# Optimization experiments

Hardware: AMD Instinct MI355X
Metric: run time of the kernel (lower is better)

Reference implementation:

```python
import jax, jax.numpy as jnp
import numpy as np

N_NODES = 10000; N_EDGES = 320000; D_NODE = 32; D_RAD = 8; D_SPH = 9
DIMS = (1, 3, 5); OFFS = (0, 1, 4); NI = 3; M = 8; HD = 16; LAT = 64; NL = 2; EPS = 1e-5
IDX = np.repeat(np.arange(NI), DIMS)  # irrep index per spherical-harmonic component
WN_ENV = NI * M            # 24  MakeWeightedChannels weight_numel
WN_LIN = NI * M * M        # 192 per-layer e3nn Linear weight_numel
GEN_W = LAT + WN_ENV + WN_LIN  # 280
WN_FIN = NI * M * LAT      # 1536 final Linear weight_numel


def _mlp(x, W):
    # ScalarMLPFunction with no hidden layers: linear with 1/sqrt(fan_in) normalization
    return x @ (W * (W.shape[0] ** -0.5))


def _ln(x, g, b):
    mu = jnp.mean(x, -1, keepdims=True)
    v = jnp.var(x, -1, keepdims=True)
    return (x - mu) * jax.lax.rsqrt(v + EPS) * g + b


def _so3_norm(x):  # x [N, M, 9]; per-irrep RMS over channel norms (equivariant)
    out = []
    for o, d in zip(OFFS, DIMS):
        blk = x[..., o:o + d]
        n2 = jnp.mean(jnp.sum(blk * blk, -1), -1)  # [N]
        out.append(blk * jax.lax.rsqrt(n2 + EPS)[:, None, None])
    return jnp.concatenate(out, -1)


def _env_weighter(sph, w):  # sph [E,9], w [E, NI*M] -> [E, M, 9]
    wf = w.reshape(-1, NI, M)[:, IDX, :]  # [E, 9, M]
    return jnp.einsum('ed,edm->emd', sph, wf)


def _eq_linear(x, w):  # x [E, Min, 9], w [E, NI, Min, Mout] -> [E, Mout, 9]
    sc = x.shape[1] ** -0.5  # e3nn path normalization 1/sqrt(fan_in)
    out = [jnp.einsum('eid,eio->eod', x[..., o:o + d], w[:, k]) * sc
           for k, (o, d) in enumerate(zip(OFFS, DIMS))]
    return jnp.concatenate(out, -1)


def _scatter_softmax(w, seg, n):  # w [E, M], softmax grouped by seg along axis 0
    m = jax.ops.segment_max(w, seg, num_segments=n)
    e = jnp.exp(w - m[seg])
    s = jax.ops.segment_sum(e, seg, num_segments=n)
    return e / (s[seg] + 1e-12)


def setup_inputs():
    key = jax.random.key(0)
    ks = jax.random.split(key, 24)
    f = jnp.float32
    inp = {}
    inp['node_attr'] = jax.random.normal(ks[0], (N_NODES, D_NODE), f)
    inp['phi'] = jax.random.normal(ks[1], (N_EDGES, D_RAD), f)
    inp['sph'] = jax.random.normal(ks[2], (N_EDGES, D_SPH), f)
    inp['edge_length'] = jax.random.uniform(ks[3], (N_EDGES,), f)
    inp['W_node'] = jax.random.normal(ks[4], (D_NODE, LAT), f)
    inp['W_center_node'] = jax.random.normal(ks[5], (D_NODE, LAT), f)
    inp['W_concat_node'] = jax.random.normal(ks[6], (2 * LAT, LAT), f)
    inp['W_edge'] = jax.random.normal(ks[7], (D_RAD, LAT), f)
    inp['ln0_g'] = jnp.ones((LAT,), f); inp['ln0_b'] = jnp.zeros((LAT,), f)
    inp['lne_g'] = jnp.ones((LAT,), f); inp['lne_b'] = jnp.zeros((LAT,), f)
    inp['W_tcat'] = jax.random.normal(ks[8], (2 * LAT + D_RAD, LAT), f)
    inp['W_temb0'] = jax.random.normal(ks[9], (LAT, WN_ENV), f)
    inp['W_hjemb0'] = jax.random.normal(ks[10], (LAT, WN_ENV), f)
    inp['W_rs'] = jax.random.normal(ks[11], (NL, LAT, GEN_W), f)
    inp['W_hj'] = jax.random.normal(ks[12], (NL, LAT, GEN_W), f)
    inp['lnl_g'] = jnp.ones((NL, LAT), f); inp['lnl_b'] = jnp.zeros((NL, LAT), f)
    inp['W_q'] = jax.random.normal(ks[13], (NL, LAT, M * HD), f)
    inp['W_k'] = jax.random.normal(ks[14], (NL, LAT, M * HD), f)
    inp['W_hemb'] = jax.random.normal(ks[15], (LAT, WN_FIN), f)
    inp['W_tij_emb'] = jax.random.normal(ks[16], (LAT, LAT), f)
    inp['edge_center'] = jax.random.randint(ks[17], (N_EDGES,), 0, N_NODES)
    inp['edge_neighbor'] = jax.random.randint(ks[18], (N_EDGES,), 0, N_NODES)
    inp['num_nodes'] = N_NODES
    return inp


def reference(node_attr, phi, sph, edge_length, W_node, W_center_node, W_concat_node, W_edge,
              ln0_g, ln0_b, lne_g, lne_b, W_tcat, W_temb0, W_hjemb0,
              W_rs, W_hj, lnl_g, lnl_b, W_q, W_k, W_hemb, W_tij_emb,
              edge_center, edge_neighbor, num_nodes):
    N = num_nodes
    # ---- init_features ----
    pn = node_attr @ W_node                              # [N, LAT]
    pe = pn[edge_neighbor] * (phi @ W_edge)              # [E, LAT]
    m_node = jax.ops.segment_sum(pe, edge_center, num_segments=N)
    pc = node_attr @ W_center_node
    h = _ln(jnp.concatenate([pc, m_node], -1) @ W_concat_node, ln0_g, ln0_b)
    t_cat = jnp.concatenate([h[edge_center], h[edge_neighbor], phi], -1)
    t_ij = _ln(_mlp(t_cat, W_tcat), lne_g, lne_b)
    w0 = _mlp(t_ij, W_temb0) * _mlp(h[edge_neighbor], W_hjemb0)   # [E, WN_ENV]
    X = _so3_norm(jax.ops.segment_sum(_env_weighter(sph, w0), edge_center, num_segments=N))  # [N, M, 9]
    # ---- interaction layers ----
    for l in range(NL):
        h_j = h[edge_neighbor]
        env = (t_ij @ W_rs[l]) * _mlp(h_j, W_hj[l])      # [E, GEN_W]
        h = _ln(h + jax.ops.segment_sum(env[:, :LAT], edge_center, num_segments=N), lnl_g[l], lnl_b[l])
        # NOTE: source does not advance w_index after first narrow -> slices overlap (faithful)
        d_sph = _env_weighter(sph, env[:, :WN_ENV])
        w_lin = env[:, WN_ENV:WN_ENV + WN_LIN].reshape(-1, NI, M, M)
        d_eq = _eq_linear(X[edge_neighbor], w_lin)
        x = d_sph + d_eq                                  # [E, M, 9]
        Q = (t_ij @ W_q[l]).reshape(-1, M, HD)
        K = (h_j @ W_k[l]).reshape(-1, M, HD)
        att = jnp.sum(Q * K, -1) * 4.0                    # math.isqrt(16)=4, MULTIPLIED as in source
        a = _scatter_softmax(att, edge_center, N)
        X = _so3_norm(X + jax.ops.segment_sum(x * a[:, :, None], edge_center, num_segments=N))
    # ---- readout ----
    w = _mlp(h, W_hemb).reshape(-1, NI, M, LAT)
    Xo = _eq_linear(X, w)                                 # [N, LAT, 9]
    node_out = jnp.concatenate([Xo[..., o:o + d].reshape(-1, LAT * d) for o, d in zip(OFFS, DIMS)], -1)
    edge_out = _mlp(t_ij, W_tij_emb)                      # [E, LAT]
    return node_out, edge_out
```

## Files before the change

### kernel.cpp

```cpp
#include <hip/hip_runtime.h>
#include <hip/hip_bf16.h>

#define N_NODES 10000
#define N_EDGES 320000
#define D_NODE 32
#define D_RAD 8
#define D_SPH 9
#define LAT 64
#define NHEAD 8
#define NL 2
#define GEN_W 280
#define WN_ENV 24

#define RS136 0.08574929257125442f
#define RS8   0.35355339059327373f

static_assert(N_EDGES % 4 == 0, "edge quads");

__device__ __forceinline__ int irrep_of(int d){ return (d==0)?0:((d<4)?1:2); }

__device__ __forceinline__ float wave_sum(float v){
  #pragma unroll
  for (int off=32; off; off>>=1) v += __shfl_xor(v, off);
  return v;
}

__device__ __forceinline__ void atomicMaxF(float* addr, float v){
  if (v >= 0.f) atomicMax((int*)addr, __float_as_int(v));
  else          atomicMin((unsigned int*)addr, __float_as_uint(v));
}

__device__ __forceinline__ float f4g(const float4& v, int i){
  return (i==0)?v.x:((i==1)?v.y:((i==2)?v.z:v.w));
}

__global__ void fill_neg_inf(float* p, int n){
  int i = blockIdx.x*blockDim.x + threadIdx.x;
  if (i < n) p[i] = __uint_as_float(0xff800000u);
}

__global__ void k_node_proj(const float* __restrict__ na,
                            const float* __restrict__ Wn,
                            const float* __restrict__ Wc,
                            float* __restrict__ pn, float* __restrict__ pc){
  int idx = blockIdx.x*blockDim.x + threadIdx.x;
  int n = idx >> 6, j = idx & 63;
  if (n >= N_NODES) return;
  float an = 0.f, ac = 0.f;
  #pragma unroll
  for (int k = 0; k < D_NODE; k++){
    float a = na[n*D_NODE + k];
    an += a * Wn[k*LAT + j];
    ac += a * Wc[k*LAT + j];
  }
  pn[idx] = an; pc[idx] = ac;
}

__global__ void __launch_bounds__(256,4) k_edge_msg(const float* __restrict__ phi,
                           const float* __restrict__ We,
                           const int* __restrict__ ec, const int* __restrict__ en,
                           const float* __restrict__ pn, float* __restrict__ mnode){
  __shared__ float swe[8*64];
  for (int i = threadIdx.x; i < 8*64; i += 256) swe[i] = We[i];
  __syncthreads();
  const int j = threadIdx.x & 63;
  int wid = blockIdx.x*4 + (threadIdx.x >> 6);
  int nw  = gridDim.x*4;
  for (int p = wid; p < N_EDGES/4; p += nw){
    const int eb = p*4;
    int4 cv = *(const int4*)(ec + eb);
    int4 nv = *(const int4*)(en + eb);
    int c0 = __builtin_amdgcn_readfirstlane(cv.x);
    int c1 = __builtin_amdgcn_readfirstlane(cv.y);
    int c2 = __builtin_amdgcn_readfirstlane(cv.z);
    int c3 = __builtin_amdgcn_readfirstlane(cv.w);
    int n0 = __builtin_amdgcn_readfirstlane(nv.x);
    int n1 = __builtin_amdgcn_readfirstlane(nv.y);
    int n2 = __builtin_amdgcn_readfirstlane(nv.z);
    int n3 = __builtin_amdgcn_readfirstlane(nv.w);
    const float4* ph = (const float4*)(phi + (long)eb*D_RAD);
    float d0=0.f, d1=0.f, d2=0.f, d3=0.f;
    #pragma unroll
    for (int kk = 0; kk < 2; kk++){
      float4 p0=ph[kk], p1=ph[2+kk], p2=ph[4+kk], p3=ph[6+kk];
      #pragma unroll
      for (int i = 0; i < 4; i++){
        float u = swe[(kk*4+i)*64 + j];
        d0+=f4g(p0,i)*u; d1+=f4g(p1,i)*u; d2+=f4g(p2,i)*u; d3+=f4g(p3,i)*u;
      }
    }
    atomicAdd(&mnode[(long)c0*LAT + j], pn[(long)n0*LAT + j] * d0);
    atomicAdd(&mnode[(long)c1*LAT + j], pn[(long)n1*LAT + j] * d1);
    atomicAdd(&mnode[(long)c2*LAT + j], pn[(long)n2*LAT + j] * d2);
    atomicAdd(&mnode[(long)c3*LAT + j], pn[(long)n3*LAT + j] * d3);
  }
}

__global__ void k_node_h(const float* __restrict__ pc, const float* __restrict__ mnode,
                         const float* __restrict__ Wcat,
                         const float* __restrict__ g, const float* __restrict__ b,
                         float* __restrict__ h0, float* __restrict__ h){
  int n = blockIdx.x*(blockDim.x >> 6) + (threadIdx.x >> 6);
  int j = threadIdx.x & 63;
  if (n >= N_NODES) return;
  float acc = 0.f;
  for (int k = 0; k < LAT; k++) acc += pc[n*LAT + k] * Wcat[k*LAT + j];
  for (int k = 0; k < LAT; k++) acc += mnode[n*LAT + k] * Wcat[(LAT + k)*LAT + j];
  float mu = wave_sum(acc) * (1.f/64.f);
  float va = wave_sum(acc*acc) * (1.f/64.f) - mu*mu;
  float v = (acc - mu) * rsqrtf(va + 1e-5f) * g[j] + b[j];
  h0[n*LAT + j] = v; h[n*LAT + j] = v;
}

__global__ void __launch_bounds__(256) k_pre0(const float* __restrict__ h0,
                       const float* __restrict__ Wtcat, const float* __restrict__ Wh0,
                       float* __restrict__ P0){
  __shared__ float sw[64*152];
  for (int i = threadIdx.x; i < 64*152; i += 256){
    int k = i / 152, c = i - k*152;
    float v;
    if (c < 64)       v = Wtcat[k*64 + c] * RS136;
    else if (c < 128) v = Wtcat[(64 + k)*64 + (c - 64)] * RS136;
    else              v = Wh0[k*24 + (c - 128)] * 0.125f;
    sw[i] = v;
  }
  __syncthreads();
  const int j = threadIdx.x & 63;
  int wid = blockIdx.x*4 + (threadIdx.x >> 6);
  int nw = gridDim.x*4;
  for (int n = wid; n < N_NODES; n += nw){
    const float4* xp = (const float4*)(h0 + (long)n*LAT);
    float a0=0.f, a1=0.f, a2=0.f;
    #pragma unroll 2
    for (int kk = 0; kk < 16; kk++){
      float4 xv = xp[kk];
      #pragma unroll
      for (int i = 0; i < 4; i++){
        float xi = f4g(xv, i);
        const float* w = sw + (kk*4+i)*152;
        a0 += xi * w[j];
        a1 += xi * w[64 + j];
        if (j < 24) a2 += xi * w[128 + j];
      }
    }
    P0[(long)n*152 + j] = a0;
    P0[(long)n*152 + 64 + j] = a1;
    if (j < 24) P0[(long)n*152 + 128 + j] = a2;
  }
}

template<int C>
__global__ void __launch_bounds__(256) k_node_mm(const float* __restrict__ in,
    const float* __restrict__ W, int ldw, float scale, float* __restrict__ out){
  __shared__ float sw[64*C];
  for (int i = threadIdx.x; i < 64*C; i += 256){
    int k = i / C, c = i - k*C;
    sw[i] = W[k*ldw + c] * scale;
  }
  __syncthreads();
  const int j = threadIdx.x & 63;
  constexpr int G = (C + 63)/64;
  int wid = blockIdx.x*4 + (threadIdx.x >> 6);
  int nw = gridDim.x*4;
  for (int n = wid; n < N_NODES; n += nw){
    const float4* xp = (const float4*)(in + (long)n*LAT);
    float acc[G];
    #pragma unroll
    for (int g = 0; g < G; g++) acc[g] = 0.f;
    #pragma unroll 2
    for (int kk = 0; kk < 16; kk++){
      float4 xv = xp[kk];
      #pragma unroll
      for (int i = 0; i < 4; i++){
        float xi = f4g(xv, i);
        int k = kk*4 + i;
        #pragma unroll
        for (int g = 0; g < G; g++){
          int c = g*64 + j;
          if (c < C) acc[g] += xi * sw[k*C + c];
        }
      }
    }
    #pragma unroll
    for (int g = 0; g < G; g++){
      int c = g*64 + j;
      if (c < C) out[(long)n*C + c] = acc[g];
    }
  }
}

__global__ void __launch_bounds__(256,5) k_tij(
    const float* __restrict__ P0, const float* __restrict__ phi,
    const float* __restrict__ sph,
    const float* __restrict__ Wtcat,
    const float* __restrict__ lg, const float* __restrict__ lb,
    const float* __restrict__ Wtij, const float* __restrict__ Wt0,
    const int* __restrict__ ec, const int* __restrict__ en,
    float* __restrict__ T, float* __restrict__ Xacc,
    float* __restrict__ edge_out){
  __shared__ float sW3[8*64];
  __shared__ float swij[64*64];
  __shared__ float sw0[64*24];
  __shared__ float tst[4][4][64];
  for (int i = threadIdx.x; i < 8*64;  i += 256) sW3[i] = Wtcat[128*64 + i] * RS136;
  for (int i = threadIdx.x; i < 64*64; i += 256) swij[i] = Wtij[i];
  for (int i = threadIdx.x; i < 64*24; i += 256) sw0[i] = Wt0[i];
  __syncthreads();
  const int j = threadIdx.x & 63, lw = threadIdx.x >> 6;
  const float gj = lg[j], bj = lb[j];
  const int jc = (j < 24) ? j : 0;
  int wid = blockIdx.x*4 + lw;
  int nw  = gridDim.x*4;
  for (int p = wid; p < N_EDGES/4; p += nw){
    const int eb = p*4;
    int4 cv = *(const int4*)(ec + eb);
    int4 nv = *(const int4*)(en + eb);
    int ccs[4], nns[4];
    ccs[0] = __builtin_amdgcn_readfirstlane(cv.x);
    ccs[1] = __builtin_amdgcn_readfirstlane(cv.y);
    ccs[2] = __builtin_amdgcn_readfirstlane(cv.z);
    ccs[3] = __builtin_amdgcn_readfirstlane(cv.w);
    nns[0] = __builtin_amdgcn_readfirstlane(nv.x);
    nns[1] = __builtin_amdgcn_readfirstlane(nv.y);
    nns[2] = __builtin_amdgcn_readfirstlane(nv.z);
    nns[3] = __builtin_amdgcn_readfirstlane(nv.w);
    float a[4];
    #pragma unroll
    for (int x = 0; x < 4; x++)
      a[x] = P0[(long)ccs[x]*152 + j] + P0[(long)nns[x]*152 + 64 + j];
    const float4* ph = (const float4*)(phi + (long)eb*D_RAD);
    #pragma unroll
    for (int kk = 0; kk < 2; kk++){
      float4 p0=ph[kk], p1=ph[2+kk], p2=ph[4+kk], p3=ph[6+kk];
      #pragma unroll
      for (int i = 0; i < 4; i++){
        float u = sW3[(kk*4+i)*64 + j];
        a[0]+=f4g(p0,i)*u; a[1]+=f4g(p1,i)*u; a[2]+=f4g(p2,i)*u; a[3]+=f4g(p3,i)*u;
      }
    }
    #pragma unroll
    for (int x = 0; x < 4; x++){
      float acc = a[x];
      float mu = wave_sum(acc) * (1.f/64.f);
      float va = wave_sum(acc*acc) * (1.f/64.f) - mu*mu;
      float t = (acc - mu) * rsqrtf(va + 1e-5f) * gj + bj;
      T[(long)(eb+x)*LAT + j] = t;
      tst[lw][x][j] = t;
    }
    float hh[4];
    #pragma unroll
    for (int x = 0; x < 4; x++) hh[x] = P0[(long)nns[x]*152 + 128 + jc];
    float eo[4]={0,0,0,0}, av[4]={0,0,0,0};
    #pragma unroll 2
    for (int kk = 0; kk < 16; kk++){
      float4 tv0 = *(const float4*)&tst[lw][0][kk*4];
      float4 tv1 = *(const float4*)&tst[lw][1][kk*4];
      float4 tv2 = *(const float4*)&tst[lw][2][kk*4];
      float4 tv3 = *(const float4*)&tst[lw][3][kk*4];
      #pragma unroll
      for (int i = 0; i < 4; i++){
        float u = swij[(kk*4+i)*64 + j];
        float w = sw0[(kk*4+i)*24 + jc];
        eo[0]+=f4g(tv0,i)*u; av[0]+=f4g(tv0,i)*w;
        eo[1]+=f4g(tv1,i)*u; av[1]+=f4g(tv1,i)*w;
        eo[2]+=f4g(tv2,i)*u; av[2]+=f4g(tv2,i)*w;
        eo[3]+=f4g(tv3,i)*u; av[3]+=f4g(tv3,i)*w;
      }
    }
    float w0s[4];
    #pragma unroll
    for (int x = 0; x < 4; x++){
      edge_out[(long)(eb+x)*LAT + j] = eo[x] * 0.125f;
      w0s[x] = av[x] * hh[x] * 0.125f;
    }
    #pragma unroll
    for (int x = 0; x < 4; x++){
      #pragma unroll
      for (int rep = 0; rep < 2; rep++){
        int tt = j + rep*64;
        int m = tt/9, d = tt - (tt/9)*9;
        int wi = (tt < 72) ? (irrep_of(d)*NHEAD + m) : 0;
        float wv = __shfl(w0s[x], wi);
        if (tt < 72){
          atomicAdd(&Xacc[ccs[x]*72 + tt], sph[(long)(eb+x)*D_SPH + d] * wv);
        }
      }
    }
  }
}

__global__ void k_node_X0(const float* __restrict__ Xacc, float* __restrict__ X){
  int n = blockIdx.x*(blockDim.x >> 6) + (threadIdx.x >> 6);
  int j = threadIdx.x & 63;
  if (n >= N_NODES) return;
  float x0 = Xacc[n*72 + j];
  float x1 = (j < 8) ? Xacc[n*72 + 64 + j] : 0.f;
  float s0 = 0.f, s1 = 0.f, s2 = 0.f;
  { int d = j % 9; int k3 = irrep_of(d);
    if (k3 == 0) s0 = x0*x0; else if (k3 == 1) s1 = x0*x0; else s2 = x0*x0; }
  if (j < 8){ int d = (64 + j) % 9; int k3 = irrep_of(d);
    if (k3 == 0) s0 += x1*x1; else if (k3 == 1) s1 += x1*x1; else s2 += x1*x1; }
  s0 = wave_sum(s0); s1 = wave_sum(s1); s2 = wave_sum(s2);
  float sa = rsqrtf(s0*0.125f + 1e-5f), sb = rsqrtf(s1*0.125f + 1e-5f), sc = rsqrtf(s2*0.125f + 1e-5f);
  { int d = j % 9; int k3 = irrep_of(d);
    X[n*72 + j] = x0 * (k3==0 ? sa : (k3==1 ? sb : sc)); }
  if (j < 8){ int d = (64 + j) % 9; int k3 = irrep_of(d);
    X[n*72 + 64 + j] = x1 * (k3==0 ? sa : (k3==1 ? sb : sc)); }
}

__global__ void __launch_bounds__(256,4) k_att(const float* __restrict__ T, const float* __restrict__ Hk,
                     const float* __restrict__ Wq,
                     const int* __restrict__ ec, const int* __restrict__ en,
                     float* __restrict__ att, float* __restrict__ attmax){
  __shared__ float sq[64*128];
  for (int i = threadIdx.x; i < 64*128; i += 256) sq[i] = Wq[i];
  __syncthreads();
  const int j = threadIdx.x & 63;
  int wid = blockIdx.x*4 + (threadIdx.x >> 6);
  int nw  = gridDim.x*4;
  for (int p = wid; p < N_EDGES/4; p += nw){
    const int eb = p*4;
    int4 cv = *(const int4*)(ec + eb);
    int4 nv = *(const int4*)(en + eb);
    int ccs[4], nns[4];
    ccs[0] = __builtin_amdgcn_readfirstlane(cv.x);
    ccs[1] = __builtin_amdgcn_readfirstlane(cv.y);
    ccs[2] = __builtin_amdgcn_readfirstlane(cv.z);
    ccs[3] = __builtin_amdgcn_readfirstlane(cv.w);
    nns[0] = __builtin_amdgcn_readfirstlane(nv.x);
    nns[1] = __builtin_amdgcn_readfirstlane(nv.y);
    nns[2] = __builtin_amdgcn_readfirstlane(nv.z);
    nns[3] = __builtin_amdgcn_readfirstlane(nv.w);
    const float4* tp0 = (const float4*)(T + (long)(eb+0)*LAT);
    const float4* tp1 = (const float4*)(T + (long)(eb+1)*LAT);
    const float4* tp2 = (const float4*)(T + (long)(eb+2)*LAT);
    const float4* tp3 = (const float4*)(T + (long)(eb+3)*LAT);
    float qa[4]={0,0,0,0}, qb[4]={0,0,0,0};
    #pragma unroll 2
    for (int kk = 0; kk < 16; kk++){
      float4 tv[4] = {tp0[kk], tp1[kk], tp2[kk], tp3[kk]};
      const float* wq = sq + (kk*4)*128 + j;
      #pragma unroll
      for (int i = 0; i < 4; i++){
        float q0 = wq[i*128], q1 = wq[i*128 + 64];
        #pragma unroll
        for (int x = 0; x < 4; x++){
          float tx = f4g(tv[x], i);
          qa[x] += tx*q0; qb[x] += tx*q1;
        }
      }
    }
    float pa[4], pb[4];
    #pragma unroll
    for (int x = 0; x < 4; x++){
      pa[x] = qa[x] * Hk[(long)nns[x]*128 + j];
      pb[x] = qb[x] * Hk[(long)nns[x]*128 + 64 + j];
    }
    #pragma unroll
    for (int off = 8; off; off >>= 1){
      #pragma unroll
      for (int x = 0; x < 4; x++){
        pa[x] += __shfl_xor(pa[x], off);
        pb[x] += __shfl_xor(pb[x], off);
      }
    }
    if ((j & 15) == 0){
      int m = j >> 4;
      #pragma unroll
      for (int x = 0; x < 4; x++){
        float A = 4.f*pa[x], B = 4.f*pb[x];
        att[(long)(eb+x)*NHEAD + m] = A;
        att[(long)(eb+x)*NHEAD + 4 + m] = B;
        atomicMaxF(&attmax[ccs[x]*NHEAD + m], A);
        atomicMaxF(&attmax[ccs[x]*NHEAD + 4 + m], B);
      }
    }
  }
}

__global__ void __launch_bounds__(1024,4) k_env(
    const float* __restrict__ T, const float* __restrict__ Hw,
    const float* __restrict__ X,
    const float* __restrict__ Wrs,
    const float* __restrict__ sph,
    const float* __restrict__ att, const float* __restrict__ attmax,
    const int* __restrict__ ec, const int* __restrict__ en,
    float* __restrict__ hacc, float* __restrict__ asum,
    float* __restrict__ Xacc){
  __shared__ float srs[64*216];
  __shared__ float senv[16][4][216];
  __shared__ float sxn[16][4][80];
  __shared__ float sev[16][32];
  for (int i = threadIdx.x; i < 64*216; i += 1024){
    int k = i / 216, c = i - k*216;
    srs[i] = Wrs[k*GEN_W + c];
  }
  __syncthreads();
  const int j = threadIdx.x & 63, lw = threadIdx.x >> 6;
  int wid = blockIdx.x*16 + lw;
  int nw  = gridDim.x*16;
  for (int p = wid; p < N_EDGES/4; p += nw){
    const int eb = p*4;
    int4 cv = *(const int4*)(ec + eb);
    int4 nv = *(const int4*)(en + eb);
    int ccs[4], nns[4];
    ccs[0] = __builtin_amdgcn_readfirstlane(cv.x);
    ccs[1] = __builtin_amdgcn_readfirstlane(cv.y);
    ccs[2] = __builtin_amdgcn_readfirstlane(cv.z);
    ccs[3] = __builtin_amdgcn_readfirstlane(cv.w);
    nns[0] = __builtin_amdgcn_readfirstlane(nv.x);
    nns[1] = __builtin_amdgcn_readfirstlane(nv.y);
    nns[2] = __builtin_amdgcn_readfirstlane(nv.z);
    nns[3] = __builtin_amdgcn_readfirstlane(nv.w);
    #pragma unroll
    for (int x = 0; x < 4; x++){
      const float* Xr = X + (long)nns[x]*72;
      sxn[lw][x][j] = Xr[j];
      if (j < 8) sxn[lw][x][64 + j] = Xr[64 + j];
    }
    const float4* tp0 = (const float4*)(T + (long)(eb+0)*LAT);
    const float4* tp1 = (const float4*)(T + (long)(eb+1)*LAT);
    const float4* tp2 = (const float4*)(T + (long)(eb+2)*LAT);
    const float4* tp3 = (const float4*)(T + (long)(eb+3)*LAT);
    float4 aT[4];
    #pragma unroll
    for (int x = 0; x < 4; x++) aT[x] = make_float4(0.f,0.f,0.f,0.f);
    if (j < 54){
      #pragma unroll 2
      for (int kk = 0; kk < 16; kk++){
        float4 tv[4] = {tp0[kk], tp1[kk], tp2[kk], tp3[kk]};
        #pragma unroll
        for (int i = 0; i < 4; i++){
          const float4 r4 = *(const float4*)(srs + (kk*4+i)*216 + j*4);
          #pragma unroll
          for (int x = 0; x < 4; x++){
            float tx = f4g(tv[x], i);
            aT[x].x += tx*r4.x; aT[x].y += tx*r4.y; aT[x].z += tx*r4.z; aT[x].w += tx*r4.w;
          }
        }
      }
      #pragma unroll
      for (int x = 0; x < 4; x++){
        const float4 hw4 = *(const float4*)(Hw + (long)nns[x]*216 + j*4);
        float4 ev4;
        ev4.x = aT[x].x * hw4.x;
        ev4.y = aT[x].y * hw4.y;
        ev4.z = aT[x].z * hw4.z;
        ev4.w = aT[x].w * hw4.w;
        *(float4*)&senv[lw][x][j*4] = ev4;
      }
    }
    if (j < 32){
      int x = j >> 3, m = j & 7;
      int cc = ccs[x];
      float ev = __expf(att[(long)(eb+x)*NHEAD + m] - attmax[cc*NHEAD + m]);
      sev[lw][j] = ev;
      atomicAdd(&asum[cc*NHEAD + m], ev);
    }
    #pragma unroll
    for (int x = 0; x < 4; x++){
      atomicAdd(&hacc[ccs[x]*LAT + j], senv[lw][x][j]);
    }
    #pragma unroll
    for (int x = 0; x < 4; x++){
      const long e = eb + x;
      const int cc = ccs[x];
      #pragma unroll
      for (int rep = 0; rep < 2; rep++){
        int tt = j + rep*64;
        if (tt < 72){
          int m = tt/9, d = tt - m*9, k3 = irrep_of(d);
          float ds = sph[e*D_SPH + d] * senv[lw][x][k3*8 + m];
          float dq = 0.f;
          #pragma unroll
          for (int i = 0; i < 8; i++) dq += sxn[lw][x][i*9 + d] * senv[lw][x][24 + k3*64 + i*8 + m];
          float val = (ds + dq*RS8) * sev[lw][x*8 + m];
          atomicAdd(&Xacc[cc*72 + tt], val);
        }
      }
    }
  }
}

__global__ void k_node_upd(const float* __restrict__ hacc, const float* __restrict__ attsum,
                           const float* __restrict__ Xacc,
                           const float* __restrict__ lg, const float* __restrict__ lb,
                           float* __restrict__ h, float* __restrict__ X){
  int n = blockIdx.x*(blockDim.x >> 6) + (threadIdx.x >> 6);
  int j = threadIdx.x & 63;
  if (n >= N_NODES) return;
  float hv = h[n*LAT + j] + hacc[n*LAT + j];
  float mu = wave_sum(hv) * (1.f/64.f);
  float va = wave_sum(hv*hv) * (1.f/64.f) - mu*mu;
  h[n*LAT + j] = (hv - mu) * rsqrtf(va + 1e-5f) * lg[j] + lb[j];

  float x0, x1 = 0.f;
  float s0 = 0.f, s1 = 0.f, s2 = 0.f;
  { int m = j/9, d = j - m*9;
    x0 = X[n*72 + j] + Xacc[n*72 + j] / (attsum[n*NHEAD + m] + 1e-12f);
    int k3 = irrep_of(d);
    if (k3 == 0) s0 = x0*x0; else if (k3 == 1) s1 = x0*x0; else s2 = x0*x0; }
  if (j < 8){ int tt = 64 + j; int m = tt/9, d = tt - m*9;
    x1 = X[n*72 + tt] + Xacc[n*72 + tt] / (attsum[n*NHEAD + m] + 1e-12f);
    int k3 = irrep_of(d);
    if (k3 == 0) s0 += x1*x1; else if (k3 == 1) s1 += x1*x1; else s2 += x1*x1; }
  s0 = wave_sum(s0); s1 = wave_sum(s1); s2 = wave_sum(s2);
  float sa = rsqrtf(s0*0.125f + 1e-5f), sb = rsqrtf(s1*0.125f + 1e-5f), sc = rsqrtf(s2*0.125f + 1e-5f);
  { int d = j % 9; int k3 = irrep_of(d);
    X[n*72 + j] = x0 * (k3==0 ? sa : (k3==1 ? sb : sc)); }
  if (j < 8){ int d = (64 + j) % 9; int k3 = irrep_of(d);
    X[n*72 + 64 + j] = x1 * (k3==0 ? sa : (k3==1 ? sb : sc)); }
}

__global__ void k_node_out(const float* __restrict__ h, const float* __restrict__ X,
                           const float* __restrict__ Whemb,
                           float* __restrict__ out){
  __shared__ float sx[4][72];
  int n = blockIdx.x*(blockDim.x >> 6) + (threadIdx.x >> 6);
  int j = threadIdx.x & 63;
  int lw = threadIdx.x >> 6;
  if (n >= N_NODES) return;
  float hv = h[n*LAT + j];
  float wv[24];
  #pragma unroll
  for (int i = 0; i < 24; i++) wv[i] = 0.f;
  #pragma unroll 4
  for (int c = 0; c < LAT; c++){
    float hc = __shfl(hv, c);
    #pragma unroll
    for (int ki = 0; ki < 24; ki++)
      wv[ki] += hc * Whemb[c*1536 + ki*64 + j];
  }
  sx[lw][j] = X[n*72 + j];
  if (j < 8) sx[lw][64 + j] = X[n*72 + 64 + j];
  #pragma unroll
  for (int d = 0; d < 9; d++){
    int k3 = irrep_of(d);
    float acc = 0.f;
    #pragma unroll
    for (int i = 0; i < 8; i++) acc += sx[lw][i*9 + d] * wv[k3*8 + i];
    acc *= 0.125f * RS8;
    int pos;
    if (d == 0)      pos = n*576 + j;
    else if (d < 4)  pos = n*576 + 64  + j*3 + (d - 1);
    else             pos = n*576 + 256 + j*5 + (d - 4);
    out[pos] = acc;
  }
}

static const long O_T    = 0;
static const long O_ATT  = 20480000;
static const long O_H0   = 23040000;
static const long O_H    = 23680000;
static const long O_X    = 24320000;
static const long O_XACC = 25040000;
static const long O_HACC = 25760000;
static const long O_AMAX = 26400000;
static const long O_ASUM = 26480000;

extern "C" void kernel_launch(void* const* d_in, const int* in_sizes, int n_in,
                              void* d_out, int out_size, void* d_ws, size_t ws_size,
                              hipStream_t stream) {
  const float* na    = (const float*)d_in[0];
  const float* phi   = (const float*)d_in[1];
  const float* sph   = (const float*)d_in[2];
  const float* Wn    = (const float*)d_in[4];
  const float* Wc    = (const float*)d_in[5];
  const float* Wcat  = (const float*)d_in[6];
  const float* We    = (const float*)d_in[7];
  const float* ln0g  = (const float*)d_in[8];
  const float* ln0b  = (const float*)d_in[9];
  const float* lneg  = (const float*)d_in[10];
  const float* lneb  = (const float*)d_in[11];
  const float* Wtcat = (const float*)d_in[12];
  const float* Wt0   = (const float*)d_in[13];
  const float* Wh0   = (const float*)d_in[14];
  const float* Wrs   = (const float*)d_in[15];
  const float* Whj   = (const float*)d_in[16];
  const float* lnlg  = (const float*)d_in[17];
  const float* lnlb  = (const float*)d_in[18];
  const float* Wq    = (const float*)d_in[19];
  const float* Wk    = (const float*)d_in[20];
  const float* Whemb = (const float*)d_in[21];
  const float* Wtij  = (const float*)d_in[22];
  const int* ec = (const int*)d_in[23];
  const int* en = (const int*)d_in[24];

  float* ws   = (float*)d_ws;
  float* T    = ws + O_T;
  float* att  = ws + O_ATT;
  float* h0   = ws + O_H0;
  float* h    = ws + O_H;
  float* X    = ws + O_X;
  float* Xacc = ws + O_XACC;
  float* hacc = ws + O_HACC;
  float* amax = ws + O_AMAX;
  float* asum = ws + O_ASUM;
  float* pn   = att;
  float* pc   = att + 640000;
  float* mn   = att + 1280000;
  float* P0   = att;

  float* out      = (float*)d_out;
  float* edge_out = out + (long)N_NODES*576;
  float* Hk = out;
  float* Hw = out + 1280000;

  hipMemsetAsync(mn,   0, 640000*sizeof(float), stream);
  hipMemsetAsync(Xacc, 0, 720000*sizeof(float), stream);

  k_node_proj<<<(N_NODES*64)/256, 256, 0, stream>>>(na, Wn, Wc, pn, pc);
  k_edge_msg<<<1024, 256, 0, stream>>>(phi, We, ec, en, pn, mn);
  k_node_h<<<N_NODES/4, 256, 0, stream>>>(pc, mn, Wcat, ln0g, ln0b, h0, h);
  k_pre0<<<256, 256, 0, stream>>>(h0, Wtcat, Wh0, P0);
  k_tij<<<1024, 256, 0, stream>>>(P0, phi, sph, Wtcat, lneg, lneb, Wtij, Wt0,
                                  ec, en, T, Xacc, edge_out);
  k_node_X0<<<N_NODES/4, 256, 0, stream>>>(Xacc, X);

  for (int l = 0; l < NL; l++){
    hipMemsetAsync(hacc, 0, 640000*sizeof(float), stream);
    hipMemsetAsync(Xacc, 0, 720000*sizeof(float), stream);
    hipMemsetAsync(asum, 0, 80000*sizeof(float), stream);
    fill_neg_inf<<<(80000 + 255)/256, 256, 0, stream>>>(amax, 80000);

    k_node_mm<128><<<512, 256, 0, stream>>>(h, Wk + l*64*128, 128, 1.f, Hk);
    k_node_mm<216><<<512, 256, 0, stream>>>(h, Whj + (long)l*64*GEN_W, GEN_W, 0.125f, Hw);
    k_att<<<1024, 256, 0, stream>>>(T, Hk, Wq + l*64*128, ec, en, att, amax);
    k_env<<<256, 1024, 0, stream>>>(T, Hw, X, Wrs + (long)l*64*GEN_W, sph,
                                    att, amax, ec, en, hacc, asum, Xacc);
    k_node_upd<<<N_NODES/4, 256, 0, stream>>>(hacc, asum, Xacc, lnlg + l*64, lnlb + l*64, h, X);
  }

  k_node_out<<<N_NODES/4, 256, 0, stream>>>(h, X, Whemb, out);
}
```

Measured before the change: 1.841 ms.

## Fold accumulator resets into node kernels, vectorize shared weights, hoist gathers

The per-layer memsets and the fill kernel are dropped, and the accumulators (Xacc, hacc, asum, amax) are zeroed or reset to -inf inside the node-update kernels that last read them. Shared-memory weight tiles in k_tij and k_att are repacked as float4 so each lane does one wide LDS read instead of four scalar reads. Global gathers (Hw, Hk, sph, att, attmax, P0) are issued earlier to overlap their latency with compute. The k_env senv layout is padded so the scatter step indexes directly without per-element division. This trades fewer launches and memory operations for more register pressure and a subtle dependence on reset ordering.

```diff
diff --git a/kernel.cpp b/kernel.cpp
--- a/kernel.cpp
+++ b/kernel.cpp
@@ -32,11 +32,6 @@
 
 __device__ __forceinline__ float f4g(const float4& v, int i){
   return (i==0)?v.x:((i==1)?v.y:((i==2)?v.z:v.w));
-}
-
-__global__ void fill_neg_inf(float* p, int n){
-  int i = blockIdx.x*blockDim.x + threadIdx.x;
-  if (i < n) p[i] = __uint_as_float(0xff800000u);
 }
 
 __global__ void k_node_proj(const float* __restrict__ na,
@@ -198,13 +193,27 @@
     const int* __restrict__ ec, const int* __restrict__ en,
     float* __restrict__ T, float* __restrict__ Xacc,
     float* __restrict__ edge_out){
-  __shared__ float sW3[8*64];
-  __shared__ float swij[64*64];
-  __shared__ float sw0[64*24];
+  __shared__ float4 sW34[2*64];
+  __shared__ float4 swij4[16*64];
+  __shared__ float4 sw04[16*24];
   __shared__ float tst[4][4][64];
-  for (int i = threadIdx.x; i < 8*64;  i += 256) sW3[i] = Wtcat[128*64 + i] * RS136;
-  for (int i = threadIdx.x; i < 64*64; i += 256) swij[i] = Wtij[i];
-  for (int i = threadIdx.x; i < 64*24; i += 256) sw0[i] = Wt0[i];
+  for (int i = threadIdx.x; i < 2*64; i += 256){
+    int kk = i >> 6, j2 = i & 63;
+    sW34[i] = make_float4(Wtcat[(128+4*kk+0)*64 + j2]*RS136,
+                          Wtcat[(128+4*kk+1)*64 + j2]*RS136,
+                          Wtcat[(128+4*kk+2)*64 + j2]*RS136,
+                          Wtcat[(128+4*kk+3)*64 + j2]*RS136);
+  }
+  for (int i = threadIdx.x; i < 16*64; i += 256){
+    int kk = i >> 6, j2 = i & 63;
+    swij4[i] = make_float4(Wtij[(4*kk+0)*64 + j2], Wtij[(4*kk+1)*64 + j2],
+                           Wtij[(4*kk+2)*64 + j2], Wtij[(4*kk+3)*64 + j2]);
+  }
+  for (int i = threadIdx.x; i < 16*24; i += 256){
+    int kk = i / 24, c = i - kk*24;
+    sw04[i] = make_float4(Wt0[(4*kk+0)*24 + c], Wt0[(4*kk+1)*24 + c],
+                          Wt0[(4*kk+2)*24 + c], Wt0[(4*kk+3)*24 + c]);
+  }
   __syncthreads();
   const int j = threadIdx.x & 63, lw = threadIdx.x >> 6;
   const float gj = lg[j], bj = lb[j];
@@ -224,17 +233,20 @@
     nns[1] = __builtin_amdgcn_readfirstlane(nv.y);
     nns[2] = __builtin_amdgcn_readfirstlane(nv.z);
     nns[3] = __builtin_amdgcn_readfirstlane(nv.w);
-    float a[4];
-    #pragma unroll
-    for (int x = 0; x < 4; x++)
-      a[x] = P0[(long)ccs[x]*152 + j] + P0[(long)nns[x]*152 + 64 + j];
+    float a[4], hh[4];
+    #pragma unroll
+    for (int x = 0; x < 4; x++){
+      a[x]  = P0[(long)ccs[x]*152 + j] + P0[(long)nns[x]*152 + 64 + j];
+      hh[x] = P0[(long)nns[x]*152 + 128 + jc];
+    }
     const float4* ph = (const float4*)(phi + (long)eb*D_RAD);
     #pragma unroll
     for (int kk = 0; kk < 2; kk++){
       float4 p0=ph[kk], p1=ph[2+kk], p2=ph[4+kk], p3=ph[6+kk];
+      float4 u4 = sW34[kk*64 + j];
       #pragma unroll
       for (int i = 0; i < 4; i++){
-        float u = sW3[(kk*4+i)*64 + j];
+        float u = f4g(u4, i);
         a[0]+=f4g(p0,i)*u; a[1]+=f4g(p1,i)*u; a[2]+=f4g(p2,i)*u; a[3]+=f4g(p3,i)*u;
       }
     }
@@ -247,9 +259,6 @@
       T[(long)(eb+x)*LAT + j] = t;
       tst[lw][x][j] = t;
     }
-    float hh[4];
-    #pragma unroll
-    for (int x = 0; x < 4; x++) hh[x] = P0[(long)nns[x]*152 + 128 + jc];
     float eo[4]={0,0,0,0}, av[4]={0,0,0,0};
     #pragma unroll 2
     for (int kk = 0; kk < 16; kk++){
@@ -257,10 +266,11 @@
       float4 tv1 = *(const float4*)&tst[lw][1][kk*4];
       float4 tv2 = *(const float4*)&tst[lw][2][kk*4];
       float4 tv3 = *(const float4*)&tst[lw][3][kk*4];
+      float4 u4 = swij4[kk*64 + j];
+      float4 w4 = sw04[kk*24 + jc];
       #pragma unroll
       for (int i = 0; i < 4; i++){
-        float u = swij[(kk*4+i)*64 + j];
-        float w = sw0[(kk*4+i)*24 + jc];
+        float u = f4g(u4, i), w = f4g(w4, i);
         eo[0]+=f4g(tv0,i)*u; av[0]+=f4g(tv0,i)*w;
         eo[1]+=f4g(tv1,i)*u; av[1]+=f4g(tv1,i)*w;
         eo[2]+=f4g(tv2,i)*u; av[2]+=f4g(tv2,i)*w;
@@ -289,7 +299,9 @@
   }
 }
 
-__global__ void k_node_X0(const float* __restrict__ Xacc, float* __restrict__ X){
+__global__ void k_node_X0(float* __restrict__ Xacc, float* __restrict__ X,
+                          float* __restrict__ hacc, float* __restrict__ asum,
+                          float* __restrict__ amax){
   int n = blockIdx.x*(blockDim.x >> 6) + (threadIdx.x >> 6);
   int j = threadIdx.x & 63;
   if (n >= N_NODES) return;
@@ -306,14 +318,24 @@
     X[n*72 + j] = x0 * (k3==0 ? sa : (k3==1 ? sb : sc)); }
   if (j < 8){ int d = (64 + j) % 9; int k3 = irrep_of(d);
     X[n*72 + 64 + j] = x1 * (k3==0 ? sa : (k3==1 ? sb : sc)); }
+  Xacc[n*72 + j] = 0.f;
+  if (j < 8) Xacc[n*72 + 64 + j] = 0.f;
+  hacc[n*LAT + j] = 0.f;
+  if (j < 8){ asum[n*NHEAD + j] = 0.f; amax[n*NHEAD + j] = __uint_as_float(0xff800000u); }
 }
 
 __global__ void __launch_bounds__(256,4) k_att(const float* __restrict__ T, const float* __restrict__ Hk,
                      const float* __restrict__ Wq,
                      const int* __restrict__ ec, const int* __restrict__ en,
                      float* __restrict__ att, float* __restrict__ attmax){
-  __shared__ float sq[64*128];
-  for (int i = threadIdx.x; i < 64*128; i += 256) sq[i] = Wq[i];
+  __shared__ float4 sqa[16*64], sqb[16*64];
+  for (int i = threadIdx.x; i < 16*64; i += 256){
+    int kk = i >> 6, j2 = i & 63;
+    sqa[i] = make_float4(Wq[(4*kk+0)*128 + j2], Wq[(4*kk+1)*128 + j2],
+                         Wq[(4*kk+2)*128 + j2], Wq[(4*kk+3)*128 + j2]);
+    sqb[i] = make_float4(Wq[(4*kk+0)*128 + 64 + j2], Wq[(4*kk+1)*128 + 64 + j2],
+                         Wq[(4*kk+2)*128 + 64 + j2], Wq[(4*kk+3)*128 + 64 + j2]);
+  }
   __syncthreads();
   const int j = threadIdx.x & 63;
   int wid = blockIdx.x*4 + (threadIdx.x >> 6);
@@ -331,6 +353,12 @@
     nns[1] = __builtin_amdgcn_readfirstlane(nv.y);
     nns[2] = __builtin_amdgcn_readfirstlane(nv.z);
     nns[3] = __builtin_amdgcn_readfirstlane(nv.w);
+    float ha[4], hb[4];
+    #pragma unroll
+    for (int x = 0; x < 4; x++){
+      ha[x] = Hk[(long)nns[x]*128 + j];
+      hb[x] = Hk[(long)nns[x]*128 + 64 + j];
+    }
     const float4* tp0 = (const float4*)(T + (long)(eb+0)*LAT);
     const float4* tp1 = (const float4*)(T + (long)(eb+1)*LAT);
     const float4* tp2 = (const float4*)(T + (long)(eb+2)*LAT);
@@ -339,10 +367,11 @@
     #pragma unroll 2
     for (int kk = 0; kk < 16; kk++){
       float4 tv[4] = {tp0[kk], tp1[kk], tp2[kk], tp3[kk]};
-      const float* wq = sq + (kk*4)*128 + j;
+      float4 wa = sqa[kk*64 + j];
+      float4 wb = sqb[kk*64 + j];
       #pragma unroll
       for (int i = 0; i < 4; i++){
-        float q0 = wq[i*128], q1 = wq[i*128 + 64];
+        float q0 = f4g(wa, i), q1 = f4g(wb, i);
         #pragma unroll
         for (int x = 0; x < 4; x++){
           float tx = f4g(tv[x], i);
@@ -352,10 +381,7 @@
     }
     float pa[4], pb[4];
     #pragma unroll
-    for (int x = 0; x < 4; x++){
-      pa[x] = qa[x] * Hk[(long)nns[x]*128 + j];
-      pb[x] = qb[x] * Hk[(long)nns[x]*128 + 64 + j];
-    }
+    for (int x = 0; x < 4; x++){ pa[x] = qa[x]*ha[x]; pb[x] = qb[x]*hb[x]; }
     #pragma unroll
     for (int off = 8; off; off >>= 1){
       #pragma unroll
@@ -388,7 +414,7 @@
     float* __restrict__ hacc, float* __restrict__ asum,
     float* __restrict__ Xacc){
   __shared__ float srs[64*216];
-  __shared__ float senv[16][4][216];
+  __shared__ float senv[16][4][240];
   __shared__ float sxn[16][4][80];
   __shared__ float sev[16][32];
   for (int i = threadIdx.x; i < 64*216; i += 1024){
@@ -397,6 +423,13 @@
   }
   __syncthreads();
   const int j = threadIdx.x & 63, lw = threadIdx.x >> 6;
+  int wpos = 0;
+  if (j < 54){
+    int c0 = 4*j;
+    wpos = (c0 < 24) ? c0 : 24 + ((c0-24) >> 6)*72 + ((c0-24) & 63);
+  }
+  const int d0 = j - (j/9)*9, m0 = j/9;
+  const int d1 = 1 + j, m1 = 7;
   int wid = blockIdx.x*16 + lw;
   int nw  = gridDim.x*16;
   for (int p = wid; p < N_EDGES/4; p += nw){
@@ -412,11 +445,22 @@
     nns[1] = __builtin_amdgcn_readfirstlane(nv.y);
     nns[2] = __builtin_amdgcn_readfirstlane(nv.z);
     nns[3] = __builtin_amdgcn_readfirstlane(nv.w);
-    #pragma unroll
-    for (int x = 0; x < 4; x++){
+    float4 hw4[4];
+    float sp0[4], sp1[4];
+    float attp = 0.f, amaxp = 0.f;
+    #pragma unroll
+    for (int x = 0; x < 4; x++){
+      if (j < 54) hw4[x] = *(const float4*)(Hw + (long)nns[x]*216 + j*4);
+      sp0[x] = sph[(long)(eb+x)*D_SPH + d0];
+      if (j < 8) sp1[x] = sph[(long)(eb+x)*D_SPH + d1];
       const float* Xr = X + (long)nns[x]*72;
       sxn[lw][x][j] = Xr[j];
       if (j < 8) sxn[lw][x][64 + j] = Xr[64 + j];
+    }
+    if (j < 32){
+      int x = j >> 3, m = j & 7;
+      attp  = att[(long)(eb+x)*NHEAD + m];
+      amaxp = attmax[ccs[x]*NHEAD + m];
     }
     const float4* tp0 = (const float4*)(T + (long)(eb+0)*LAT);
     const float4* tp1 = (const float4*)(T + (long)(eb+1)*LAT);
@@ -441,21 +485,19 @@
       }
       #pragma unroll
       for (int x = 0; x < 4; x++){
-        const float4 hw4 = *(const float4*)(Hw + (long)nns[x]*216 + j*4);
         float4 ev4;
-        ev4.x = aT[x].x * hw4.x;
-        ev4.y = aT[x].y * hw4.y;
-        ev4.z = aT[x].z * hw4.z;
-        ev4.w = aT[x].w * hw4.w;
-        *(float4*)&senv[lw][x][j*4] = ev4;
+        ev4.x = aT[x].x * hw4[x].x;
+        ev4.y = aT[x].y * hw4[x].y;
+        ev4.z = aT[x].z * hw4[x].z;
+        ev4.w = aT[x].w * hw4[x].w;
+        *(float4*)&senv[lw][x][wpos] = ev4;
       }
     }
     if (j < 32){
       int x = j >> 3, m = j & 7;
-      int cc = ccs[x];
-      float ev = __expf(att[(long)(eb+x)*NHEAD + m] - attmax[cc*NHEAD + m]);
+      float ev = __expf(attp - amaxp);
       sev[lw][j] = ev;
-      atomicAdd(&asum[cc*NHEAD + m], ev);
+      atomicAdd(&asum[ccs[x]*NHEAD + m], ev);
     }
     #pragma unroll
     for (int x = 0; x < 4; x++){
@@ -463,27 +505,31 @@
     }
     #pragma unroll
     for (int x = 0; x < 4; x++){
-      const long e = eb + x;
       const int cc = ccs[x];
-      #pragma unroll
-      for (int rep = 0; rep < 2; rep++){
-        int tt = j + rep*64;
-        if (tt < 72){
-          int m = tt/9, d = tt - m*9, k3 = irrep_of(d);
-          float ds = sph[e*D_SPH + d] * senv[lw][x][k3*8 + m];
-          float dq = 0.f;
-          #pragma unroll
-          for (int i = 0; i < 8; i++) dq += sxn[lw][x][i*9 + d] * senv[lw][x][24 + k3*64 + i*8 + m];
-          float val = (ds + dq*RS8) * sev[lw][x*8 + m];
-          atomicAdd(&Xacc[cc*72 + tt], val);
-        }
-      }
-    }
-  }
-}
-
-__global__ void k_node_upd(const float* __restrict__ hacc, const float* __restrict__ attsum,
-                           const float* __restrict__ Xacc,
+      {
+        int k3 = irrep_of(d0);
+        float ds = sp0[x] * senv[lw][x][k3*8 + m0];
+        float dq = 0.f;
+        #pragma unroll
+        for (int i = 0; i < 8; i++) dq += sxn[lw][x][i*9 + d0] * senv[lw][x][24 + k3*72 + i*8 + m0];
+        float val = (ds + dq*RS8) * sev[lw][x*8 + m0];
+        atomicAdd(&Xacc[cc*72 + j], val);
+      }
+      if (j < 8){
+        int k3 = irrep_of(d1);
+        float ds = sp1[x] * senv[lw][x][k3*8 + m1];
+        float dq = 0.f;
+        #pragma unroll
+        for (int i = 0; i < 8; i++) dq += sxn[lw][x][i*9 + d1] * senv[lw][x][24 + k3*72 + i*8 + m1];
+        float val = (ds + dq*RS8) * sev[lw][x*8 + m1];
+        atomicAdd(&Xacc[cc*72 + 64 + j], val);
+      }
+    }
+  }
+}
+
+__global__ void k_node_upd(float* __restrict__ hacc, float* __restrict__ attsum,
+                           float* __restrict__ Xacc, float* __restrict__ amax,
                            const float* __restrict__ lg, const float* __restrict__ lb,
                            float* __restrict__ h, float* __restrict__ X){
   int n = blockIdx.x*(blockDim.x >> 6) + (threadIdx.x >> 6);
@@ -510,6 +556,10 @@
     X[n*72 + j] = x0 * (k3==0 ? sa : (k3==1 ? sb : sc)); }
   if (j < 8){ int d = (64 + j) % 9; int k3 = irrep_of(d);
     X[n*72 + 64 + j] = x1 * (k3==0 ? sa : (k3==1 ? sb : sc)); }
+  Xacc[n*72 + j] = 0.f;
+  if (j < 8) Xacc[n*72 + 64 + j] = 0.f;
+  hacc[n*LAT + j] = 0.f;
+  if (j < 8){ attsum[n*NHEAD + j] = 0.f; amax[n*NHEAD + j] = __uint_as_float(0xff800000u); }
 }
 
 __global__ void k_node_out(const float* __restrict__ h, const float* __restrict__ X,
@@ -615,20 +665,16 @@
   k_pre0<<<256, 256, 0, stream>>>(h0, Wtcat, Wh0, P0);
   k_tij<<<1024, 256, 0, stream>>>(P0, phi, sph, Wtcat, lneg, lneb, Wtij, Wt0,
                                   ec, en, T, Xacc, edge_out);
-  k_node_X0<<<N_NODES/4, 256, 0, stream>>>(Xacc, X);
+  k_node_X0<<<N_NODES/4, 256, 0, stream>>>(Xacc, X, hacc, asum, amax);
 
   for (int l = 0; l < NL; l++){
-    hipMemsetAsync(hacc, 0, 640000*sizeof(float), stream);
-    hipMemsetAsync(Xacc, 0, 720000*sizeof(float), stream);
-    hipMemsetAsync(asum, 0, 80000*sizeof(float), stream);
-    fill_neg_inf<<<(80000 + 255)/256, 256, 0, stream>>>(amax, 80000);
-
     k_node_mm<128><<<512, 256, 0, stream>>>(h, Wk + l*64*128, 128, 1.f, Hk);
     k_node_mm<216><<<512, 256, 0, stream>>>(h, Whj + (long)l*64*GEN_W, GEN_W, 0.125f, Hw);
     k_att<<<1024, 256, 0, stream>>>(T, Hk, Wq + l*64*128, ec, en, att, amax);
     k_env<<<256, 1024, 0, stream>>>(T, Hw, X, Wrs + (long)l*64*GEN_W, sph,
                                     att, amax, ec, en, hacc, asum, Xacc);
-    k_node_upd<<<N_NODES/4, 256, 0, stream>>>(hacc, asum, Xacc, lnlg + l*64, lnlb + l*64, h, X);
+    k_node_upd<<<N_NODES/4, 256, 0, stream>>>(hacc, asum, Xacc, amax,
+                                              lnlg + l*64, lnlb + l*64, h, X);
   }
 
   k_node_out<<<N_NODES/4, 256, 0, stream>>>(h, X, Whemb, out);
```

Result: no change. 1.863 ms (+1.2%).
